# Kernel tuning notes

Measured on AMD Instinct MI355X. Metric: run time of the kernel, lower is better.

The kernel has to match this reference:

```python
import jax, jax.numpy as jnp
import numpy as np
from jax import lax

B, MEL, T, I, H, C = 8, 64, 512, 128, 128, 20


def setup_inputs() -> dict:
    key = jax.random.key(0)
    ks = jax.random.split(key, 64)
    ki = iter(range(64))

    def w(shape):
        return jax.random.normal(ks[next(ki)], shape, dtype=jnp.float32) * 0.05

    inp = {"x": jax.random.normal(ks[next(ki)], (B, MEL, T), dtype=jnp.float32)}
    # (name, out_features, in_features) for every nn.Linear in the module
    lins = [
        ("in", I, MEL), ("out", C, H),
        ("ii", H, I), ("hi", H, H), ("if", H, I), ("hf", H, H),
        ("ig", H, I), ("hg", H, H), ("io", H, I), ("ho", H, H),
        ("xo", H, I), ("q", H, H), ("k", H, H), ("v", H, 1), ("ao", 1, H),
    ]
    for n, o, i in lins:
        inp[f"W_{n}"] = w((o, i))
        inp[f"b_{n}"] = w((o,))
    return inp


def _lin(z, W, b):
    return z @ W.T + b


def _forward(x, W_in, b_in, W_out, b_out, W_ii, b_ii, W_hi, b_hi, W_if, b_if,
             W_hf, b_hf, W_ig, b_ig, W_hg, b_hg, W_io, b_io, W_ho, b_ho,
             W_xo, b_xo, W_q, b_q, W_k, b_k, W_v, b_v, W_ao, b_ao):
    Bsz = x.shape[0]
    Hd = W_ii.shape[0]
    scale = float(Hd) ** 0.5
    # (B, MEL, T) -> (B, T, MEL) -> input_proj -> (B, T, I) -> (T, B, I) for scan
    xp = _lin(jnp.transpose(x, (0, 2, 1)), W_in, b_in)
    xs = jnp.transpose(xp, (1, 0, 2))

    c0 = jnp.zeros((Bsz, Hd), dtype=x.dtype)
    h0 = jnp.zeros((Bsz, Hd), dtype=x.dtype)

    def step(carry, x_t):
        c, h = carry
        i = jax.nn.sigmoid(_lin(x_t, W_ii, b_ii) + _lin(h, W_hi, b_hi))
        f = jax.nn.sigmoid(_lin(x_t, W_if, b_if) + _lin(h, W_hf, b_hf))
        g = jnp.tanh(_lin(x_t, W_ig, b_ig) + _lin(h, W_hg, b_hg))
        o = jax.nn.sigmoid(_lin(x_t, W_io, b_io) + _lin(h, W_ho, b_ho))
        c_new = f * c + i * g
        x_o = jax.nn.sigmoid(_lin(x_t, W_xo, b_xo))
        # attention: q, k are (B, H); scores are rank-1 outer product (B, H, H)
        q = _lin(x_o, W_q, b_q)
        k = _lin(c_new, W_k, b_k)
        # v_proj: Linear(1, H) applied to o.unsqueeze(2) -> (B, H, H)
        v = o[:, :, None] * W_v[None, None, :, 0] + b_v[None, None, :]
        attn = jax.nn.softmax(q[:, :, None] * k[:, None, :] / scale, axis=-1)
        out = jnp.einsum('bij,bjk->bik', attn, v)  # (B, H, H)
        # attention_out_proj: Linear(H, 1) then squeeze -> new hidden (B, H)
        h_new = jnp.einsum('bij,j->bi', out, W_ao[0]) + b_ao[0]
        y = _lin(h_new, W_out, b_out)  # (B, C)
        return (c_new, h_new), y

    _, ys = lax.scan(step, (c0, h0), xs)  # ys: (T, B, C)
    return jnp.transpose(ys, (1, 2, 0))  # (B, C, T)


def reference(x, W_in, b_in, W_out, b_out, W_ii, b_ii, W_hi, b_hi, W_if, b_if,
              W_hf, b_hf, W_ig, b_ig, W_hg, b_hg, W_io, b_io, W_ho, b_ho,
              W_xo, b_xo, W_q, b_q, W_k, b_k, W_v, b_v, W_ao, b_ao):
    return _forward(x, W_in, b_in, W_out, b_out, W_ii, b_ii, W_hi, b_hi,
                    W_if, b_if, W_hf, b_hf, W_ig, b_ig, W_hg, b_hg,
                    W_io, b_io, W_ho, b_ho, W_xo, b_xo, W_q, b_q,
                    W_k, b_k, W_v, b_v, W_ao, b_ao)
```

## Files before the change

kernel.cpp:

```cpp
#include <hip/hip_runtime.h>
#include <hip/hip_bf16.h>

#define BB 8
#define MELN 64
#define TSN 512
#define HHN 128
#define CCN 20

#define OFF_WINT  0
#define OFF_WT    8192
#define OFF_RS    (OFF_WT + 10*16384)
#define OFF_XPRE  (OFF_RS + 512)
#define OFF_AQ    (OFF_XPRE + BB*TSN*512)
#define OFF_HALL  (OFF_AQ + BB*TSN*128)
#define OFF_APRE  (OFF_HALL + BB*TSN*128)

typedef _Float16 hf2 __attribute__((ext_vector_type(2)));

__device__ __forceinline__ float rcp_f(float x) { return __builtin_amdgcn_rcpf(x); }
__device__ __forceinline__ float sigm_f(float x) { return rcp_f(1.0f + __expf(-x)); }
__device__ __forceinline__ float tanh_f(float x) { return fmaf(2.0f, rcp_f(1.0f + __expf(-2.0f * x)), -1.0f); }
__device__ __forceinline__ float sigm_p(float x) { return 1.0f / (1.0f + __expf(-x)); }

#if __has_builtin(__builtin_amdgcn_fdot2)
__device__ __forceinline__ float dot2f(hf2 a, hf2 b, float c) {
  return __builtin_amdgcn_fdot2(a, b, c, false);
}
#else
__device__ __forceinline__ float dot2f(hf2 a, hf2 b, float c) {
  return fmaf((float)a.x, (float)b.x, fmaf((float)a.y, (float)b.y, c));
}
#endif

__device__ __forceinline__ hf2 mk2(float a, float b) {
  hf2 v; v.x = (_Float16)a; v.y = (_Float16)b; return v;
}
__device__ __forceinline__ unsigned pk2(float a, float b) {
  return __builtin_bit_cast(unsigned, __builtin_amdgcn_cvt_pkrtz(a, b));
}
__device__ __forceinline__ hf2 u2h(unsigned u) { return __builtin_bit_cast(hf2, u); }

#if __has_builtin(__builtin_amdgcn_update_dpp)
template <int CTRL>
__device__ __forceinline__ float dppadd(float x) {
  int v = __builtin_amdgcn_update_dpp(0, __builtin_bit_cast(int, x), CTRL, 0xf, 0xf, true);
  return x + __builtin_bit_cast(float, v);
}
__device__ __forceinline__ float wsum64(float x) {
  x = dppadd<0x111>(x);
  x = dppadd<0x112>(x);
  x = dppadd<0x114>(x);
  x = dppadd<0x118>(x);
  x = dppadd<0x142>(x);
  x = dppadd<0x143>(x);
  return x;
}
#else
__device__ __forceinline__ float wsum64(float x) {
  x += __shfl_xor(x, 1);  x += __shfl_xor(x, 2);  x += __shfl_xor(x, 4);
  x += __shfl_xor(x, 8);  x += __shfl_xor(x, 16); x += __shfl_xor(x, 32);
  return x;
}
#endif

__global__ void k_prep(const float* __restrict__ W_in, const float* __restrict__ W_ii,
                       const float* __restrict__ W_if, const float* __restrict__ W_ig,
                       const float* __restrict__ W_io, const float* __restrict__ W_xo,
                       const float* __restrict__ W_q,  const float* __restrict__ W_hi,
                       const float* __restrict__ W_hf, const float* __restrict__ W_hg,
                       const float* __restrict__ W_ho, float* __restrict__ ws) {
  int m = blockIdx.x;
  if (m == 11) {
    for (int idx = threadIdx.x; idx < 512; idx += blockDim.x) {
      int g = idx >> 7, r = idx & 127;
      const float* W = (g == 0) ? W_hi : (g == 1) ? W_hf : (g == 2) ? W_hg : W_ho;
      float s = 0.f;
      for (int c = 0; c < 128; ++c) s += W[r * 128 + c];
      ws[OFF_RS + r * 4 + g] = s;
    }
    return;
  }
  const float* src;
  float* dst;
  int C;
  if (m == 0) { src = W_in; dst = ws + OFF_WINT; C = 64; }
  else {
    const float* s[10] = {W_ii, W_if, W_ig, W_io, W_xo, W_q, W_hi, W_hf, W_hg, W_ho};
    src = s[m - 1];
    dst = ws + OFF_WT + (size_t)(m - 1) * 16384;
    C = 128;
  }
  int n = 128 * C;
  for (int idx = threadIdx.x; idx < n; idx += blockDim.x) {
    int r = idx / C, c = idx - r * C;
    dst[c * 128 + r] = src[idx];
  }
}

__global__ __launch_bounds__(128)
void k_xproj(const float* __restrict__ x,
             const float* __restrict__ b_in,
             const float* __restrict__ b_ii, const float* __restrict__ b_hi,
             const float* __restrict__ b_if, const float* __restrict__ b_hf,
             const float* __restrict__ b_ig, const float* __restrict__ b_hg,
             const float* __restrict__ b_io, const float* __restrict__ b_ho,
             const float* __restrict__ b_xo, const float* __restrict__ b_q,
             float* __restrict__ ws) {
  const int tid = threadIdx.x;
  const int b  = blockIdx.x >> 6;
  const int t0 = (blockIdx.x & 63) * 8;

  __shared__ __align__(16) float xsT[MELN * 8];
  __shared__ __align__(16) float xpsT[128 * 8];
  __shared__ __align__(16) float xosT[128 * 8];

  const float* WinT = ws + OFF_WINT;
  const float* WT   = ws + OFF_WT;
  float* Xpre = ws + OFF_XPRE;
  float* aq   = ws + OFF_AQ;

  #pragma unroll
  for (int k = 0; k < 4; ++k) {
    int mm = k * 16 + (tid >> 3);
    int tt = tid & 7;
    xsT[mm * 8 + tt] = x[((size_t)b * MELN + mm) * TSN + t0 + tt];
  }
  __syncthreads();

  float acc8[8];
  {
    float bi = b_in[tid];
    #pragma unroll
    for (int j = 0; j < 8; ++j) acc8[j] = bi;
  }
  for (int mI = 0; mI < MELN; ++mI) {
    float w = WinT[mI * 128 + tid];
    float4 xa = *(const float4*)&xsT[mI * 8];
    float4 xb = *(const float4*)&xsT[mI * 8 + 4];
    acc8[0] = fmaf(w, xa.x, acc8[0]); acc8[1] = fmaf(w, xa.y, acc8[1]);
    acc8[2] = fmaf(w, xa.z, acc8[2]); acc8[3] = fmaf(w, xa.w, acc8[3]);
    acc8[4] = fmaf(w, xb.x, acc8[4]); acc8[5] = fmaf(w, xb.y, acc8[5]);
    acc8[6] = fmaf(w, xb.z, acc8[6]); acc8[7] = fmaf(w, xb.w, acc8[7]);
  }
  *(float4*)&xpsT[tid * 8]     = make_float4(acc8[0], acc8[1], acc8[2], acc8[3]);
  *(float4*)&xpsT[tid * 8 + 4] = make_float4(acc8[4], acc8[5], acc8[6], acc8[7]);
  __syncthreads();

  float accg[5][8];
  {
    float bsum[5];
    bsum[0] = b_ii[tid] + b_hi[tid];
    bsum[1] = b_if[tid] + b_hf[tid];
    bsum[2] = b_ig[tid] + b_hg[tid];
    bsum[3] = b_io[tid] + b_ho[tid];
    bsum[4] = b_xo[tid];
    #pragma unroll
    for (int g = 0; g < 5; ++g)
      #pragma unroll
      for (int j = 0; j < 8; ++j) accg[g][j] = bsum[g];
  }
  for (int c = 0; c < 128; ++c) {
    const float4 xa = *(const float4*)&xpsT[c * 8];
    const float4 xb = *(const float4*)&xpsT[c * 8 + 4];
    #pragma unroll
    for (int g = 0; g < 5; ++g) {
      const float w = WT[g * 16384 + c * 128 + tid];
      accg[g][0] = fmaf(w, xa.x, accg[g][0]);
      accg[g][1] = fmaf(w, xa.y, accg[g][1]);
      accg[g][2] = fmaf(w, xa.z, accg[g][2]);
      accg[g][3] = fmaf(w, xa.w, accg[g][3]);
      accg[g][4] = fmaf(w, xb.x, accg[g][4]);
      accg[g][5] = fmaf(w, xb.y, accg[g][5]);
      accg[g][6] = fmaf(w, xb.z, accg[g][6]);
      accg[g][7] = fmaf(w, xb.w, accg[g][7]);
    }
  }
  {
    size_t base = ((size_t)b * TSN + t0) * 512;
    #pragma unroll
    for (int tt = 0; tt < 8; ++tt)
      *(float4*)&Xpre[base + (size_t)tt * 512 + tid * 4] =
          make_float4(accg[0][tt], accg[1][tt], accg[2][tt], accg[3][tt]);
  }
  {
    #pragma unroll
    for (int tt = 0; tt < 8; ++tt) xosT[tid * 8 + tt] = sigm_p(accg[4][tt]);
  }
  __syncthreads();

  float accq[8];
  {
    float bq = b_q[tid];
    #pragma unroll
    for (int j = 0; j < 8; ++j) accq[j] = bq;
  }
  for (int c = 0; c < 128; ++c) {
    const float w = WT[5 * 16384 + c * 128 + tid];
    const float4 xa = *(const float4*)&xosT[c * 8];
    const float4 xb = *(const float4*)&xosT[c * 8 + 4];
    accq[0] = fmaf(w, xa.x, accq[0]); accq[1] = fmaf(w, xa.y, accq[1]);
    accq[2] = fmaf(w, xa.z, accq[2]); accq[3] = fmaf(w, xa.w, accq[3]);
    accq[4] = fmaf(w, xb.x, accq[4]); accq[5] = fmaf(w, xb.y, accq[5]);
    accq[6] = fmaf(w, xb.z, accq[6]); accq[7] = fmaf(w, xb.w, accq[7]);
  }
  float av[8];
  #pragma unroll
  for (int tt = 0; tt < 8; ++tt) {
    av[tt] = accq[tt] * 0.08838834764831845f;
    aq[((size_t)b * TSN + t0 + tt) * 128 + tid] = av[tt];
  }

  __syncthreads();
  *(float4*)&xpsT[tid * 8]     = make_float4(av[0], av[1], av[2], av[3]);
  *(float4*)&xpsT[tid * 8 + 4] = make_float4(av[4], av[5], av[6], av[7]);
  __syncthreads();
  float accA[4][8];
  #pragma unroll
  for (int g = 0; g < 4; ++g)
    #pragma unroll
    for (int j = 0; j < 8; ++j) accA[g][j] = 0.f;
  for (int c = 0; c < 128; ++c) {
    const float4 xa = *(const float4*)&xpsT[c * 8];
    const float4 xb = *(const float4*)&xpsT[c * 8 + 4];
    #pragma unroll
    for (int g = 0; g < 4; ++g) {
      const float w = WT[(6 + g) * 16384 + c * 128 + tid];
      accA[g][0] = fmaf(w, xa.x, accA[g][0]);
      accA[g][1] = fmaf(w, xa.y, accA[g][1]);
      accA[g][2] = fmaf(w, xa.z, accA[g][2]);
      accA[g][3] = fmaf(w, xa.w, accA[g][3]);
      accA[g][4] = fmaf(w, xb.x, accA[g][4]);
      accA[g][5] = fmaf(w, xb.y, accA[g][5]);
      accA[g][6] = fmaf(w, xb.z, accA[g][6]);
      accA[g][7] = fmaf(w, xb.w, accA[g][7]);
    }
  }
  __syncthreads();
  *(float4*)&xpsT[tid * 8]     = make_float4(av[0]*av[0], av[1]*av[1], av[2]*av[2], av[3]*av[3]);
  *(float4*)&xpsT[tid * 8 + 4] = make_float4(av[4]*av[4], av[5]*av[5], av[6]*av[6], av[7]*av[7]);
  __syncthreads();
  float accB[4][8];
  #pragma unroll
  for (int g = 0; g < 4; ++g)
    #pragma unroll
    for (int j = 0; j < 8; ++j) accB[g][j] = 0.f;
  for (int c = 0; c < 128; ++c) {
    const float4 xa = *(const float4*)&xpsT[c * 8];
    const float4 xb = *(const float4*)&xpsT[c * 8 + 4];
    #pragma unroll
    for (int g = 0; g < 4; ++g) {
      const float w = WT[(6 + g) * 16384 + c * 128 + tid];
      accB[g][0] = fmaf(w, xa.x, accB[g][0]);
      accB[g][1] = fmaf(w, xa.y, accB[g][1]);
      accB[g][2] = fmaf(w, xa.z, accB[g][2]);
      accB[g][3] = fmaf(w, xa.w, accB[g][3]);
      accB[g][4] = fmaf(w, xb.x, accB[g][4]);
      accB[g][5] = fmaf(w, xb.y, accB[g][5]);
      accB[g][6] = fmaf(w, xb.z, accB[g][6]);
      accB[g][7] = fmaf(w, xb.w, accB[g][7]);
    }
  }
  {
    uint4* APre4 = (uint4*)(ws + OFF_APRE);
    #pragma unroll
    for (int tt = 0; tt < 8; ++tt) {
      uint4 u;
      u.x = pk2(accA[0][tt], accB[0][tt]);
      u.y = pk2(accA[1][tt], accB[1][tt]);
      u.z = pk2(accA[2][tt], accB[2][tt]);
      u.w = pk2(accA[3][tt], accB[3][tt]);
      APre4[((size_t)b * TSN + t0 + tt) * 128 + tid] = u;
    }
  }
}

__global__ __launch_bounds__(128, 1)
void k_scan(const float* __restrict__ W_k,  const float* __restrict__ b_k,
            const float* __restrict__ W_v,  const float* __restrict__ b_v,
            const float* __restrict__ W_ao, const float* __restrict__ b_ao,
            float* __restrict__ ws) {
  const int tid  = threadIdx.x;
  const int lane = tid & 63;
  const int wid  = tid >> 6;
  const int b    = blockIdx.x;

  __shared__ __align__(16) _Float16 ch[128];
  __shared__ __align__(16) float part[16];

  hf2 wkk2[64];
  #pragma unroll
  for (int p = 0; p < 64; ++p)
    wkk2[p] = mk2(W_k[(size_t)tid * 128 + 2 * p], W_k[(size_t)tid * 128 + 2 * p + 1]);
  const float bkr = b_k[tid];
  const float4 RSv = *(const float4*)&ws[OFF_RS + tid * 4];

  float s1 = 0.f, s2 = 0.f;
  for (int j = 0; j < 128; ++j) {
    s1 = fmaf(W_ao[j], W_v[j], s1);
    s2 = fmaf(W_ao[j], b_v[j], s2);
  }
  s2 += b_ao[0];
  const float inv128 = 0.0078125f;
  const float s1i = s1 * inv128;

  const float* Xb = ws + OFF_XPRE + (size_t)b * TSN * 512;
  const float* ab = ws + OFF_AQ   + (size_t)b * TSN * 128;
  float*       Hb = ws + OFF_HALL + (size_t)b * TSN * 128;
  const uint4* APb = (const uint4*)(ws + OFF_APRE) + (size_t)b * TSN * 128;

  const uint4* c4u = (const uint4*)ch;

  float4 X4e = *(const float4*)&Xb[tid * 4];
  float4 X4o = *(const float4*)&Xb[512 + tid * 4];
  float  are = ab[tid];
  float  aro = ab[128 + tid];
  uint4  Ae  = APb[tid];
  uint4  Ao  = APb[tid];

  float c_reg = 0.f;
  float g0 = 0.f;
  hf2   g12 = u2h(0u);

#define SCAN_STEP(T, X4v, arv, Argv)                                          \
  {                                                                           \
    const float pi = dot2f(u2h((Argv).x), g12, fmaf(g0, RSv.x, (X4v).x));     \
    const float pf = dot2f(u2h((Argv).y), g12, fmaf(g0, RSv.y, (X4v).y));     \
    const float pg = dot2f(u2h((Argv).z), g12, fmaf(g0, RSv.z, (X4v).z));     \
    const float po = dot2f(u2h((Argv).w), g12, fmaf(g0, RSv.w, (X4v).w));     \
    const float gi = sigm_f(pi);                                              \
    const float gf = sigm_f(pf);                                              \
    const float gg = tanh_f(pg);                                              \
    const float go = sigm_f(po);                                              \
    c_reg = fmaf(gf, c_reg, gi * gg);                                         \
    ch[tid] = (_Float16)c_reg;                                                \
    __syncthreads();                                       \
    float ka0 = 0.f, ka1 = 0.f, ka2 = 0.f, ka3 = 0.f;                         \
    _Pragma("unroll")                                                         \
    for (int u = 0; u < 16; ++u) {                                            \
      const uint4 cv = c4u[u];                                                \
      ka0 = dot2f(wkk2[u * 4 + 0], u2h(cv.x), ka0);                           \
      ka1 = dot2f(wkk2[u * 4 + 1], u2h(cv.y), ka1);                           \
      ka2 = dot2f(wkk2[u * 4 + 2], u2h(cv.z), ka2);                           \
      ka3 = dot2f(wkk2[u * 4 + 3], u2h(cv.w), ka3);                           \
    }                                                                         \
    const float kr = ((ka0 + ka1) + (ka2 + ka3)) + bkr;                       \
    const float kp2 = kr * kr;                                                \
    float m0 = kr, m1 = go, m2 = kp2, m3 = go * kr, m4 = go * kp2;            \
    m0 = wsum64(m0); m1 = wsum64(m1); m2 = wsum64(m2);                        \
    m3 = wsum64(m3); m4 = wsum64(m4);                                         \
    if (lane == 63) {                                                         \
      part[wid * 8 + 0] = m0; part[wid * 8 + 1] = m1;                         \
      part[wid * 8 + 2] = m2; part[wid * 8 + 3] = m3;                         \
      part[wid * 8 + 4] = m4;                                                 \
    }                                                                         \
    __syncthreads();                                \
    const float4 pa = *(const float4*)&part[0];                               \
    const float4 pb = *(const float4*)&part[8];                               \
    const float D1 = pa.x + pb.x;                                             \
    const float N0 = pa.y + pb.y;                                             \
    const float D2 = pa.z + pb.z;                                             \
    const float N1 = pa.w + pb.w;                                             \
    const float N2 = part[4] + part[12];                                      \
    const float t1 = D1 * inv128;                                             \
    g0 = fmaf(s1i, N0, s2);                                                   \
    const float gm1 = s1i * (N1 - N0 * t1);                                   \
    const float gm2 = s1i * (0.5f * N2 - (N1 * D1 + 0.5f * N0 * D2) * inv128  \
                             + N0 * t1 * t1);                                 \
    const float hn = fmaf(fmaf(gm2, (arv), gm1), (arv), g0);                  \
    Hb[(size_t)(T) * 128 + tid] = hn;                                         \
    g12 = u2h(pk2(gm1, gm2));                                                 \
            \
    {                                                                         \
      const int tx = ((T) + 2 < TSN) ? (T) + 2 : TSN - 1;                     \
      (X4v) = *(const float4*)&Xb[(size_t)tx * 512 + tid * 4];                \
      (arv) = ab[(size_t)tx * 128 + tid];                                     \
      const int ta = ((T) + 1 < TSN) ? (T) + 1 : TSN - 1;                     \
      (Argv) = APb[(size_t)ta * 128 + tid];                                   \
    }                                                                         \
  }

  for (int k = 0; k < TSN / 2; ++k) {
    SCAN_STEP(2 * k,     X4e, are, Ae);
    SCAN_STEP(2 * k + 1, X4o, aro, Ao);
  }
#undef SCAN_STEP
}

__global__ __launch_bounds__(256)
void k_out(const float* __restrict__ W_out, const float* __restrict__ b_out,
           const float* __restrict__ ws, float* __restrict__ out) {
  const int tid = threadIdx.x;
  const int b  = blockIdx.x >> 3;
  const int t0 = (blockIdx.x & 7) * 64;

  __shared__ __align__(16) float Hs[64 * 136];

  const float* Hb = ws + OFF_HALL + ((size_t)b * TSN + t0) * 128;
  for (int k = 0; k < 32; ++k) {
    const int idx = k * 256 + tid;
    Hs[(idx >> 7) * 136 + (idx & 127)] = Hb[idx];
  }
  __syncthreads();

  const int tt = tid & 63;
  const int c0 = (tid >> 6) * 5;
  for (int j = 0; j < 5; ++j) {
    const int c = c0 + j;
    float s = b_out[c];
    for (int i = 0; i < 128; ++i)
      s = fmaf(Hs[tt * 136 + i], W_out[c * 128 + i], s);
    out[((size_t)b * CCN + c) * TSN + t0 + tt] = s;
  }
}

extern "C" void kernel_launch(void* const* d_in, const int* in_sizes, int n_in,
                              void* d_out, int out_size, void* d_ws, size_t ws_size,
                              hipStream_t stream) {
  const float* x    = (const float*)d_in[0];
  const float* W_in = (const float*)d_in[1];
  const float* b_in = (const float*)d_in[2];
  const float* W_out= (const float*)d_in[3];
  const float* b_out= (const float*)d_in[4];
  const float* W_ii = (const float*)d_in[5];
  const float* b_ii = (const float*)d_in[6];
  const float* W_hi = (const float*)d_in[7];
  const float* b_hi = (const float*)d_in[8];
  const float* W_if = (const float*)d_in[9];
  const float* b_if = (const float*)d_in[10];
  const float* W_hf = (const float*)d_in[11];
  const float* b_hf = (const float*)d_in[12];
  const float* W_ig = (const float*)d_in[13];
  const float* b_ig = (const float*)d_in[14];
  const float* W_hg = (const float*)d_in[15];
  const float* b_hg = (const float*)d_in[16];
  const float* W_io = (const float*)d_in[17];
  const float* b_io = (const float*)d_in[18];
  const float* W_ho = (const float*)d_in[19];
  const float* b_ho = (const float*)d_in[20];
  const float* W_xo = (const float*)d_in[21];
  const float* b_xo = (const float*)d_in[22];
  const float* W_q  = (const float*)d_in[23];
  const float* b_q  = (const float*)d_in[24];
  const float* W_k  = (const float*)d_in[25];
  const float* b_k  = (const float*)d_in[26];
  const float* W_v  = (const float*)d_in[27];
  const float* b_v  = (const float*)d_in[28];
  const float* W_ao = (const float*)d_in[29];
  const float* b_ao = (const float*)d_in[30];

  float* ws = (float*)d_ws;
  float* out = (float*)d_out;

  k_prep<<<12, 256, 0, stream>>>(W_in, W_ii, W_if, W_ig, W_io, W_xo, W_q,
                                 W_hi, W_hf, W_hg, W_ho, ws);
  k_xproj<<<512, 128, 0, stream>>>(x, b_in, b_ii, b_hi, b_if, b_hf, b_ig, b_hg,
                                   b_io, b_ho, b_xo, b_q, ws);
  k_scan<<<BB, 128, 0, stream>>>(W_k, b_k, W_v, b_v, W_ao, b_ao, ws);
  k_out<<<BB * 8, 256, 0, stream>>>(W_out, b_out, ws, out);
}
```

Measured before the change: 509.5 us.

## Run scan with a single wavefront, two hidden rows per lane, no barriers

The recurrent scan kernel now runs one 64-lane wavefront per batch instead of two, and each lane owns two hidden units. This removes both __syncthreads per timestep and the cross-wave shared-memory partial-sum exchange. An all-lanes reduction (row DPP plus xor shuffles) replaces the lane-63 write, and a manual lgkmcnt wait replaces the barrier before reading the shared c vector. Each lane now does twice the gate and dot-product work, and register pressure rises from holding two W_k rows. The next-step loads are also moved earlier in the step.

```diff
diff --git a/kernel.cpp b/kernel.cpp
--- a/kernel.cpp
+++ b/kernel.cpp
@@ -46,17 +46,17 @@
   int v = __builtin_amdgcn_update_dpp(0, __builtin_bit_cast(int, x), CTRL, 0xf, 0xf, true);
   return x + __builtin_bit_cast(float, v);
 }
-__device__ __forceinline__ float wsum64(float x) {
-  x = dppadd<0x111>(x);
-  x = dppadd<0x112>(x);
-  x = dppadd<0x114>(x);
-  x = dppadd<0x118>(x);
-  x = dppadd<0x142>(x);
-  x = dppadd<0x143>(x);
+__device__ __forceinline__ float allsum64(float x) {
+  x = dppadd<0x121>(x);
+  x = dppadd<0x122>(x);
+  x = dppadd<0x124>(x);
+  x = dppadd<0x128>(x);
+  x += __shfl_xor(x, 16);
+  x += __shfl_xor(x, 32);
   return x;
 }
 #else
-__device__ __forceinline__ float wsum64(float x) {
+__device__ __forceinline__ float allsum64(float x) {
   x += __shfl_xor(x, 1);  x += __shfl_xor(x, 2);  x += __shfl_xor(x, 4);
   x += __shfl_xor(x, 8);  x += __shfl_xor(x, 16); x += __shfl_xor(x, 32);
   return x;
@@ -274,25 +274,30 @@
   }
 }
 
-__global__ __launch_bounds__(128, 1)
+__global__ __launch_bounds__(64, 1)
 void k_scan(const float* __restrict__ W_k,  const float* __restrict__ b_k,
             const float* __restrict__ W_v,  const float* __restrict__ b_v,
             const float* __restrict__ W_ao, const float* __restrict__ b_ao,
             float* __restrict__ ws) {
-  const int tid  = threadIdx.x;
-  const int lane = tid & 63;
-  const int wid  = tid >> 6;
-  const int b    = blockIdx.x;
-
-  __shared__ __align__(16) _Float16 ch[128];
-  __shared__ __align__(16) float part[16];
-
-  hf2 wkk2[64];
+  const int l  = threadIdx.x;
+  const int b  = blockIdx.x;
+  const int r0 = 2 * l, r1 = 2 * l + 1;
+
+  __shared__ __align__(16) unsigned ch32[64];
+
+  hf2 wk0[64], wk1[64];
   #pragma unroll
-  for (int p = 0; p < 64; ++p)
-    wkk2[p] = mk2(W_k[(size_t)tid * 128 + 2 * p], W_k[(size_t)tid * 128 + 2 * p + 1]);
-  const float bkr = b_k[tid];
-  const float4 RSv = *(const float4*)&ws[OFF_RS + tid * 4];
+  for (int q = 0; q < 32; ++q) {
+    const float4 w0 = *(const float4*)&W_k[(size_t)r0 * 128 + 4 * q];
+    const float4 w1 = *(const float4*)&W_k[(size_t)r1 * 128 + 4 * q];
+    wk0[2 * q]     = mk2(w0.x, w0.y);
+    wk0[2 * q + 1] = mk2(w0.z, w0.w);
+    wk1[2 * q]     = mk2(w1.x, w1.y);
+    wk1[2 * q + 1] = mk2(w1.z, w1.w);
+  }
+  const float bk0 = b_k[r0], bk1 = b_k[r1];
+  const float4 RS0 = *(const float4*)&ws[OFF_RS + r0 * 4];
+  const float4 RS1 = *(const float4*)&ws[OFF_RS + r1 * 4];
 
   float s1 = 0.f, s2 = 0.f;
   for (int j = 0; j < 128; ++j) {
@@ -308,80 +313,94 @@
   float*       Hb = ws + OFF_HALL + (size_t)b * TSN * 128;
   const uint4* APb = (const uint4*)(ws + OFF_APRE) + (size_t)b * TSN * 128;
 
-  const uint4* c4u = (const uint4*)ch;
-
-  float4 X4e = *(const float4*)&Xb[tid * 4];
-  float4 X4o = *(const float4*)&Xb[512 + tid * 4];
-  float  are = ab[tid];
-  float  aro = ab[128 + tid];
-  uint4  Ae  = APb[tid];
-  uint4  Ao  = APb[tid];
-
-  float c_reg = 0.f;
+  const uint4* c4u = (const uint4*)ch32;
+
+  float4 X0e = *(const float4*)&Xb[r0 * 4];
+  float4 X1e = *(const float4*)&Xb[r1 * 4];
+  float4 X0o = *(const float4*)&Xb[512 + r0 * 4];
+  float4 X1o = *(const float4*)&Xb[512 + r1 * 4];
+  float2 are = *(const float2*)&ab[r0];
+  float2 aro = *(const float2*)&ab[128 + r0];
+  uint4  A0e = APb[r0], A1e = APb[r1];
+  uint4  A0o = APb[r0], A1o = APb[r1];
+
+  float c0 = 0.f, c1 = 0.f;
   float g0 = 0.f;
   hf2   g12 = u2h(0u);
 
-#define SCAN_STEP(T, X4v, arv, Argv)                                          \
+#define SCAN_STEP(T, X0v, X1v, arv, A0v, A1v)                                 \
   {                                                                           \
-    const float pi = dot2f(u2h((Argv).x), g12, fmaf(g0, RSv.x, (X4v).x));     \
-    const float pf = dot2f(u2h((Argv).y), g12, fmaf(g0, RSv.y, (X4v).y));     \
-    const float pg = dot2f(u2h((Argv).z), g12, fmaf(g0, RSv.z, (X4v).z));     \
-    const float po = dot2f(u2h((Argv).w), g12, fmaf(g0, RSv.w, (X4v).w));     \
-    const float gi = sigm_f(pi);                                              \
-    const float gf = sigm_f(pf);                                              \
-    const float gg = tanh_f(pg);                                              \
-    const float go = sigm_f(po);                                              \
-    c_reg = fmaf(gf, c_reg, gi * gg);                                         \
-    ch[tid] = (_Float16)c_reg;                                                \
-    __syncthreads();                                       \
+    const float pi0 = dot2f(u2h((A0v).x), g12, fmaf(g0, RS0.x, (X0v).x));     \
+    const float pf0 = dot2f(u2h((A0v).y), g12, fmaf(g0, RS0.y, (X0v).y));     \
+    const float pg0 = dot2f(u2h((A0v).z), g12, fmaf(g0, RS0.z, (X0v).z));     \
+    const float po0 = dot2f(u2h((A0v).w), g12, fmaf(g0, RS0.w, (X0v).w));     \
+    const float pi1 = dot2f(u2h((A1v).x), g12, fmaf(g0, RS1.x, (X1v).x));     \
+    const float pf1 = dot2f(u2h((A1v).y), g12, fmaf(g0, RS1.y, (X1v).y));     \
+    const float pg1 = dot2f(u2h((A1v).z), g12, fmaf(g0, RS1.z, (X1v).z));     \
+    const float po1 = dot2f(u2h((A1v).w), g12, fmaf(g0, RS1.w, (X1v).w));     \
+        \
+    {                                                                         \
+      const int tx = ((T) + 2 < TSN) ? (T) + 2 : TSN - 1;                     \
+      (X0v) = *(const float4*)&Xb[(size_t)tx * 512 + r0 * 4];                 \
+      (X1v) = *(const float4*)&Xb[(size_t)tx * 512 + r1 * 4];                 \
+      const int ta = ((T) + 1 < TSN) ? (T) + 1 : TSN - 1;                     \
+      (A0v) = APb[(size_t)ta * 128 + r0];                                     \
+      (A1v) = APb[(size_t)ta * 128 + r1];                                     \
+    }                                                                         \
+    const float gi0 = sigm_f(pi0), gf0 = sigm_f(pf0);                         \
+    const float gg0 = tanh_f(pg0), go0 = sigm_f(po0);                         \
+    const float gi1 = sigm_f(pi1), gf1 = sigm_f(pf1);                         \
+    const float gg1 = tanh_f(pg1), go1 = sigm_f(po1);                         \
+    c0 = fmaf(gf0, c0, gi0 * gg0);                                            \
+    c1 = fmaf(gf1, c1, gi1 * gg1);                                            \
+    ch32[l] = __builtin_bit_cast(unsigned, mk2(c0, c1));                      \
+    __builtin_amdgcn_sched_barrier(0);                                        \
+    asm volatile("s_waitcnt lgkmcnt(0)" ::: "memory");                        \
+    __builtin_amdgcn_sched_barrier(0);                                        \
     float ka0 = 0.f, ka1 = 0.f, ka2 = 0.f, ka3 = 0.f;                         \
+    float kb0 = 0.f, kb1 = 0.f, kb2 = 0.f, kb3 = 0.f;                         \
     _Pragma("unroll")                                                         \
     for (int u = 0; u < 16; ++u) {                                            \
       const uint4 cv = c4u[u];                                                \
-      ka0 = dot2f(wkk2[u * 4 + 0], u2h(cv.x), ka0);                           \
-      ka1 = dot2f(wkk2[u * 4 + 1], u2h(cv.y), ka1);                           \
-      ka2 = dot2f(wkk2[u * 4 + 2], u2h(cv.z), ka2);                           \
-      ka3 = dot2f(wkk2[u * 4 + 3], u2h(cv.w), ka3);                           \
+      ka0 = dot2f(wk0[u * 4 + 0], u2h(cv.x), ka0);                            \
+      ka1 = dot2f(wk0[u * 4 + 1], u2h(cv.y), ka1);                            \
+      ka2 = dot2f(wk0[u * 4 + 2], u2h(cv.z), ka2);                            \
+      ka3 = dot2f(wk0[u * 4 + 3], u2h(cv.w), ka3);                            \
+      kb0 = dot2f(wk1[u * 4 + 0], u2h(cv.x), kb0);                            \
+      kb1 = dot2f(wk1[u * 4 + 1], u2h(cv.y), kb1);                            \
+      kb2 = dot2f(wk1[u * 4 + 2], u2h(cv.z), kb2);                            \
+      kb3 = dot2f(wk1[u * 4 + 3], u2h(cv.w), kb3);                            \
     }                                                                         \
-    const float kr = ((ka0 + ka1) + (ka2 + ka3)) + bkr;                       \
-    const float kp2 = kr * kr;                                                \
-    float m0 = kr, m1 = go, m2 = kp2, m3 = go * kr, m4 = go * kp2;            \
-    m0 = wsum64(m0); m1 = wsum64(m1); m2 = wsum64(m2);                        \
-    m3 = wsum64(m3); m4 = wsum64(m4);                                         \
-    if (lane == 63) {                                                         \
-      part[wid * 8 + 0] = m0; part[wid * 8 + 1] = m1;                         \
-      part[wid * 8 + 2] = m2; part[wid * 8 + 3] = m3;                         \
-      part[wid * 8 + 4] = m4;                                                 \
+    const float kr0 = ((ka0 + ka1) + (ka2 + ka3)) + bk0;                      \
+    const float kr1 = ((kb0 + kb1) + (kb2 + kb3)) + bk1;                      \
+    const float kp0 = kr0 * kr0, kp1 = kr1 * kr1;                             \
+    float m0 = kr0 + kr1;                                                     \
+    float m1 = go0 + go1;                                                     \
+    float m2 = kp0 + kp1;                                                     \
+    float m3 = fmaf(go0, kr0, go1 * kr1);                                     \
+    float m4 = fmaf(go0, kp0, go1 * kp1);                                     \
+    m0 = allsum64(m0); m1 = allsum64(m1); m2 = allsum64(m2);                  \
+    m3 = allsum64(m3); m4 = allsum64(m4);                                     \
+                  \
+    const float t1 = m0 * inv128;                                             \
+    g0 = fmaf(s1i, m1, s2);                                                   \
+    const float gm1 = s1i * (m3 - m1 * t1);                                   \
+    const float gm2 = s1i * (0.5f * m4 - (m3 * m0 + 0.5f * m1 * m2) * inv128  \
+                             + m1 * t1 * t1);                                 \
+    const float h0 = fmaf(fmaf(gm2, (arv).x, gm1), (arv).x, g0);              \
+    const float h1 = fmaf(fmaf(gm2, (arv).y, gm1), (arv).y, g0);              \
+    *(float2*)&Hb[(size_t)(T) * 128 + r0] = make_float2(h0, h1);              \
+    g12 = u2h(pk2(gm1, gm2));                                                 \
+                                \
+    {                                                                         \
+      const int tr = ((T) + 2 < TSN) ? (T) + 2 : TSN - 1;                     \
+      (arv) = *(const float2*)&ab[(size_t)tr * 128 + r0];                     \
     }                                                                         \
-    __syncthreads();                                \
-    const float4 pa = *(const float4*)&part[0];                               \
-    const float4 pb = *(const float4*)&part[8];                               \
-    const float D1 = pa.x + pb.x;                                             \
-    const float N0 = pa.y + pb.y;                                             \
-    const float D2 = pa.z + pb.z;                                             \
-    const float N1 = pa.w + pb.w;                                             \
-    const float N2 = part[4] + part[12];                                      \
-    const float t1 = D1 * inv128;                                             \
-    g0 = fmaf(s1i, N0, s2);                                                   \
-    const float gm1 = s1i * (N1 - N0 * t1);                                   \
-    const float gm2 = s1i * (0.5f * N2 - (N1 * D1 + 0.5f * N0 * D2) * inv128  \
-                             + N0 * t1 * t1);                                 \
-    const float hn = fmaf(fmaf(gm2, (arv), gm1), (arv), g0);                  \
-    Hb[(size_t)(T) * 128 + tid] = hn;                                         \
-    g12 = u2h(pk2(gm1, gm2));                                                 \
-            \
-    {                                                                         \
-      const int tx = ((T) + 2 < TSN) ? (T) + 2 : TSN - 1;                     \
-      (X4v) = *(const float4*)&Xb[(size_t)tx * 512 + tid * 4];                \
-      (arv) = ab[(size_t)tx * 128 + tid];                                     \
-      const int ta = ((T) + 1 < TSN) ? (T) + 1 : TSN - 1;                     \
-      (Argv) = APb[(size_t)ta * 128 + tid];                                   \
-    }                                                                         \
   }
 
   for (int k = 0; k < TSN / 2; ++k) {
-    SCAN_STEP(2 * k,     X4e, are, Ae);
-    SCAN_STEP(2 * k + 1, X4o, aro, Ao);
+    SCAN_STEP(2 * k,     X0e, X1e, are, A0e, A1e);
+    SCAN_STEP(2 * k + 1, X0o, X1o, aro, A0o, A1o);
   }
 #undef SCAN_STEP
 }
@@ -455,6 +474,6 @@
                                  W_hi, W_hf, W_hg, W_ho, ws);
   k_xproj<<<512, 128, 0, stream>>>(x, b_in, b_ii, b_hi, b_if, b_hf, b_ig, b_hg,
                                    b_io, b_ho, b_xo, b_q, ws);
-  k_scan<<<BB, 128, 0, stream>>>(W_k, b_k, W_v, b_v, W_ao, b_ao, ws);
+  k_scan<<<BB, 64, 0, stream>>>(W_k, b_k, W_v, b_v, W_ao, b_ao, ws);
   k_out<<<BB * 8, 256, 0, stream>>>(W_out, b_out, ws, out);
 }
```

Measured after the change: 607.9 us. 19.3% more time.
